# Kernel tuning notes

Measured on AMD Instinct MI355X. Metric: run time of the kernel, lower is better.

Reference implementation:

```python
import jax, jax.numpy as jnp
import numpy as np

N = 50000      # nodes
E = 800000     # edges (avg degree 16)
D = 128        # node_dim
H = 128        # hidden_dim
ED = 16        # edge_dim (unused by GCNConv, kept for signature fidelity)
G = 64         # graphs in batch
EPS = 1e-5     # BatchNorm eps


def setup_inputs() -> dict:
    key = jax.random.key(0)
    ks = jax.random.split(key, 16)
    s = 0.05
    inp = {
        "x": jax.random.normal(ks[0], (N, D), jnp.float32),
        "edge_index": jax.random.randint(ks[1], (2, E), 0, N, dtype=jnp.int64),
        "edge_attr": jax.random.normal(ks[2], (E, ED), jnp.float32),
        "batch": jnp.sort(jax.random.randint(ks[3], (N,), 0, G, dtype=jnp.int64)),
        # GCNConv weights/biases
        "W1": jax.random.normal(ks[4], (D, H), jnp.float32) * s,
        "b1": jnp.zeros((H,), jnp.float32),
        "W2": jax.random.normal(ks[5], (H, H), jnp.float32) * s,
        "b2": jnp.zeros((H,), jnp.float32),
        "W3": jax.random.normal(ks[6], (H, H), jnp.float32) * s,
        "b3": jnp.zeros((H,), jnp.float32),
        # BatchNorm affine params (training-mode batch stats)
        "g1": jnp.ones((H,), jnp.float32), "be1": jnp.zeros((H,), jnp.float32),
        "g2": jnp.ones((H,), jnp.float32), "be2": jnp.zeros((H,), jnp.float32),
        "g3": jnp.ones((H,), jnp.float32), "be3": jnp.zeros((H,), jnp.float32),
    }
    return inp


def reference(x, edge_index, edge_attr, batch,
              W1, b1, W2, b2, W3, b3,
              g1, be1, g2, be2, g3, be3):
    n = x.shape[0]
    src, dst = edge_index[0], edge_index[1]

    # GCN symmetric normalization with added self-loops:
    # deg[i] = 1 + in_degree(i); norm(e) = deg[src]^-1/2 * deg[dst]^-1/2
    deg = jax.ops.segment_sum(jnp.ones((src.shape[0],), x.dtype), dst,
                              num_segments=n) + 1.0
    dinv = jax.lax.rsqrt(deg)
    edge_norm = (dinv[src] * dinv[dst])[:, None]   # [E,1]
    self_norm = (dinv * dinv)[:, None]             # [N,1] self-loop weight

    def gcn(h, W, b):
        h = h @ W                                  # [N,H]
        agg = jax.ops.segment_sum(h[src] * edge_norm, dst, num_segments=n)
        return agg + h * self_norm + b

    def bn_sigmoid(h, g, b):
        m = h.mean(0)
        v = jnp.mean(jnp.square(h - m), 0)         # biased variance (torch BN)
        return jax.nn.sigmoid((h - m) * jax.lax.rsqrt(v + EPS) * g + b)

    h = bn_sigmoid(gcn(x, W1, b1), g1, be1)
    h = bn_sigmoid(gcn(h, W2, b2), g2, be2)
    h = bn_sigmoid(gcn(h, W3, b3), g3, be3)

    # global_mean_pool over graph ids
    cnt = jax.ops.segment_sum(jnp.ones((n,), h.dtype), batch, num_segments=G)
    pooled = jax.ops.segment_sum(h, batch, num_segments=G)
    return pooled / jnp.maximum(cnt, 1.0)[:, None]
```

## Files before the change

kernel.cpp:

```cpp
#include <hip/hip_runtime.h>
#include <math.h>

#define NDIM 128

typedef __attribute__((ext_vector_type(8))) short short8;
typedef __attribute__((ext_vector_type(4))) float f32x4;

__device__ __forceinline__ float sigmoidf_(float x){ return 1.0f/(1.0f + __expf(-x)); }

__device__ __forceinline__ unsigned short f2bf(float f){
  unsigned u = __float_as_uint(f);
  unsigned r = (u + 0x7fffu + ((u >> 16) & 1u)) >> 16;
  return (unsigned short)r;
}

__global__ void deg_count_k(const int* __restrict__ dst, int* __restrict__ counts, int E){
  int e = blockIdx.x*blockDim.x + threadIdx.x;
  if(e < E) atomicAdd(&counts[dst[e]], 1);
}

__global__ void scan1_k(const int* __restrict__ counts, int* __restrict__ scanned,
                        int* __restrict__ chunksums, int N){
  __shared__ int lds[256];
  int t = threadIdx.x; int idx = blockIdx.x*256 + t;
  int x = (idx < N) ? counts[idx] : 0;
  lds[t] = x; __syncthreads();
  for(int o=1;o<256;o<<=1){
    int v = (t>=o) ? lds[t-o] : 0;
    __syncthreads();
    lds[t] += v;
    __syncthreads();
  }
  if(idx < N) scanned[idx] = lds[t];
  if(t == 255) chunksums[blockIdx.x] = lds[255];
}

__global__ void scan2_k(int* __restrict__ chunksums, int nchunks){
  __shared__ int lds[256];
  int t = threadIdx.x;
  int x = (t < nchunks) ? chunksums[t] : 0;
  lds[t] = x; __syncthreads();
  for(int o=1;o<256;o<<=1){
    int v = (t>=o) ? lds[t-o] : 0;
    __syncthreads();
    lds[t] += v;
    __syncthreads();
  }
  if(t < nchunks) chunksums[t] = lds[t] - x;
}

__global__ void scan3_k(const int* __restrict__ scanned, const int* __restrict__ counts,
                        const int* __restrict__ chunksums, int* __restrict__ row_start,
                        float* __restrict__ dinv, int N){
  int i = blockIdx.x*blockDim.x + threadIdx.x;
  if(i < N){
    row_start[i] = scanned[i] - counts[i] + chunksums[i>>8];
    dinv[i] = rsqrtf(1.0f + (float)counts[i]);
  }
}

__global__ void fill_k(const int* __restrict__ src, const int* __restrict__ dst,
                       const float* __restrict__ dinv, const int* __restrict__ row_start,
                       int* __restrict__ cursor, uint2* __restrict__ csr, int E){
  int e = blockIdx.x*blockDim.x + threadIdx.x;
  if(e >= E) return;
  int d = dst[e], s = src[e];
  int pos = row_start[d] + atomicAdd(&cursor[d], 1);
  uint2 rec;
  rec.x = (unsigned)s;
  rec.y = __float_as_uint(dinv[s]*dinv[d]);
  csr[pos] = rec;
}

__global__ void bounds_k(const int* __restrict__ batch, int* __restrict__ bound, int N, int G){
  int g = threadIdx.x;
  if(g > G) return;
  int lo = 0, hi = N;
  while(lo < hi){ int mid = (lo+hi)>>1; if(batch[mid] < g) lo = mid+1; else hi = mid; }
  bound[g] = lo;
}

__global__ void wprep_k(const float* __restrict__ W0, const float* __restrict__ W1,
                        const float* __restrict__ W2, unsigned short* __restrict__ Wsw){
  int t = blockIdx.x*256 + threadIdx.x;
  if(t >= 3*16384) return;
  int l = t >> 14; int i = t & 16383;
  const float* W = (l==0) ? W0 : ((l==1) ? W1 : W2);
  int k = i >> 7, n = i & 127;
  Wsw[l*16384 + (((k>>3)*128 + n)<<3) + (k&7)] = f2bf(W[k*128+n]);
}

__global__ __launch_bounds__(256) void gemm_mfma_k(const float* __restrict__ A,
                                                   const unsigned short* __restrict__ Wsw,
                                                   unsigned short* __restrict__ Bh,
                                                   const float* __restrict__ scale,
                                                   const float* __restrict__ shift,
                                                   int N){
  __shared__ unsigned short Al[16384];
  __shared__ unsigned short Wl[16384];
  int t = threadIdx.x;
  int row0 = blockIdx.x * 128;
  bool bn = (scale != nullptr);

  #pragma unroll
  for(int i=0;i<8;i++){
    int u = t + i*256;
    *(uint4*)&Wl[u<<3] = *(const uint4*)&Wsw[u<<3];
  }
  int o = t & 15, rbase = t >> 4;
  #pragma unroll
  for(int it=0; it<8; it++){
    int r = rbase + it*16;
    int grow = row0 + r;
    float4 v0 = make_float4(0.f,0.f,0.f,0.f), v1 = v0;
    if(grow < N){
      v0 = *(const float4*)&A[grow*NDIM + o*8];
      v1 = *(const float4*)&A[grow*NDIM + o*8 + 4];
      if(bn){
        float4 sc0 = *(const float4*)&scale[o*8],   sh0 = *(const float4*)&shift[o*8];
        float4 sc1 = *(const float4*)&scale[o*8+4], sh1 = *(const float4*)&shift[o*8+4];
        v0.x = sigmoidf_(v0.x*sc0.x + sh0.x); v0.y = sigmoidf_(v0.y*sc0.y + sh0.y);
        v0.z = sigmoidf_(v0.z*sc0.z + sh0.z); v0.w = sigmoidf_(v0.w*sc0.w + sh0.w);
        v1.x = sigmoidf_(v1.x*sc1.x + sh1.x); v1.y = sigmoidf_(v1.y*sc1.y + sh1.y);
        v1.z = sigmoidf_(v1.z*sc1.z + sh1.z); v1.w = sigmoidf_(v1.w*sc1.w + sh1.w);
      }
    }
    uint4 pk;
    pk.x = (unsigned)f2bf(v0.x) | ((unsigned)f2bf(v0.y)<<16);
    pk.y = (unsigned)f2bf(v0.z) | ((unsigned)f2bf(v0.w)<<16);
    pk.z = (unsigned)f2bf(v1.x) | ((unsigned)f2bf(v1.y)<<16);
    pk.w = (unsigned)f2bf(v1.z) | ((unsigned)f2bf(v1.w)<<16);
    *(uint4*)&Al[(o*128 + r)<<3] = pk;
  }
  __syncthreads();

  int wv = t >> 6, lane = t & 63, quad = lane >> 4, l16 = lane & 15;
  int rw = (wv & 1) * 64, cw = (wv >> 1) * 64;
  f32x4 acc[4][4];
  #pragma unroll
  for(int rt=0;rt<4;rt++)
    #pragma unroll
    for(int ct=0;ct<4;ct++) acc[rt][ct] = (f32x4){0.f,0.f,0.f,0.f};

  #pragma unroll
  for(int ks=0; ks<4; ks++){
    short8 a[4], b[4];
    #pragma unroll
    for(int rt=0;rt<4;rt++)
      a[rt] = *(short8*)&Al[(((ks*4+quad)*128) + rw + rt*16 + l16) << 3];
    #pragma unroll
    for(int ct=0;ct<4;ct++)
      b[ct] = *(short8*)&Wl[(((ks*4+quad)*128) + cw + ct*16 + l16) << 3];
    #pragma unroll
    for(int rt=0;rt<4;rt++)
      #pragma unroll
      for(int ct=0;ct<4;ct++)
        acc[rt][ct] = __builtin_amdgcn_mfma_f32_16x16x32_bf16(a[rt], b[ct], acc[rt][ct], 0, 0, 0);
  }

  #pragma unroll
  for(int rt=0;rt<4;rt++){
    int gr = row0 + rw + rt*16 + quad*4;
    #pragma unroll
    for(int ct=0;ct<4;ct++){
      int col = cw + ct*16 + l16;
      #pragma unroll
      for(int reg=0;reg<4;reg++){
        if(gr + reg < N) Bh[(gr+reg)*NDIM + col] = f2bf(acc[rt][ct][reg]);
      }
    }
  }
}

__global__ void agg_k(const unsigned int* __restrict__ hb,
                      const float* __restrict__ dinv,
                      const int* __restrict__ row_start, const int* __restrict__ counts,
                      const uint2* __restrict__ csr,
                      const float* __restrict__ bias, float* __restrict__ hC, int N){
  int i = blockIdx.x;
  if(i >= N) return;
  int lane = threadIdx.x;
  int rs = row_start[i], re = rs + counts[i];
  float ax = 0.f, ay = 0.f;
  int j = rs;
  for(; j+3 < re; j += 4){
    uint2 r0 = csr[j], r1 = csr[j+1], r2 = csr[j+2], r3 = csr[j+3];
    unsigned u0 = hb[(size_t)r0.x*64 + lane];
    unsigned u1 = hb[(size_t)r1.x*64 + lane];
    unsigned u2 = hb[(size_t)r2.x*64 + lane];
    unsigned u3 = hb[(size_t)r3.x*64 + lane];
    float n0 = __uint_as_float(r0.y), n1 = __uint_as_float(r1.y);
    float n2 = __uint_as_float(r2.y), n3 = __uint_as_float(r3.y);
    ax += n0*__uint_as_float(u0<<16) + n1*__uint_as_float(u1<<16)
        + n2*__uint_as_float(u2<<16) + n3*__uint_as_float(u3<<16);
    ay += n0*__uint_as_float(u0 & 0xffff0000u) + n1*__uint_as_float(u1 & 0xffff0000u)
        + n2*__uint_as_float(u2 & 0xffff0000u) + n3*__uint_as_float(u3 & 0xffff0000u);
  }
  for(; j < re; j++){
    uint2 r0 = csr[j];
    unsigned u0 = hb[(size_t)r0.x*64 + lane];
    float n0 = __uint_as_float(r0.y);
    ax += n0*__uint_as_float(u0<<16);
    ay += n0*__uint_as_float(u0 & 0xffff0000u);
  }
  float di = dinv[i], sn = di*di;
  unsigned su = hb[(size_t)i*64 + lane];
  float2 bv = *(const float2*)&bias[lane*2];
  float2 o;
  o.x = ax + sn*__uint_as_float(su<<16)           + bv.x;
  o.y = ay + sn*__uint_as_float(su & 0xffff0000u) + bv.y;
  *(float2*)&hC[(size_t)i*NDIM + lane*2] = o;
}

__global__ void stats_k(const float* __restrict__ h, float* __restrict__ sums,
                        float* __restrict__ sumsq, int N){
  __shared__ float ls[256], lq[256];
  int t = threadIdx.x;
  int f = t & 127, half = t >> 7;
  int rowsPerBlock = (N + gridDim.x - 1)/gridDim.x;
  int r0 = blockIdx.x * rowsPerBlock;
  int r1 = min(N, r0 + rowsPerBlock);
  float s=0.f, q=0.f;
  for(int r=r0+half; r<r1; r+=2){
    float v = h[r*NDIM + f];
    s += v; q += v*v;
  }
  ls[t]=s; lq[t]=q; __syncthreads();
  if(t < 128){
    s = ls[t] + ls[t+128];
    q = lq[t] + lq[t+128];
    atomicAdd(&sums[f], s);
    atomicAdd(&sumsq[f], q);
  }
}

__global__ void finalize_k(const float* __restrict__ sums, const float* __restrict__ sumsq,
                           const float* __restrict__ g, const float* __restrict__ be,
                           float* __restrict__ scale, float* __restrict__ shift, int N){
  int f = threadIdx.x;
  float invN = 1.0f/(float)N;
  float m = sums[f]*invN;
  float var = fmaxf(sumsq[f]*invN - m*m, 0.f);
  float s = g[f]*rsqrtf(var + 1e-5f);
  scale[f] = s;
  shift[f] = be[f] - m*s;
}

#define PCH 128
__global__ __launch_bounds__(256) void pool_k(const float* __restrict__ hC,
                                              const int* __restrict__ batch,
                                              const float* __restrict__ scale,
                                              const float* __restrict__ shift,
                                              float* __restrict__ out, int N){
  int t = threadIdx.x;
  int f = t & 127, half = t >> 7;
  int r0 = blockIdx.x*PCH + half;
  int r1 = min(N, blockIdx.x*PCH + PCH);
  float sc = scale[f], sh = shift[f];
  float acc = 0.f; int cur = -1;
  for(int r = r0; r < r1; r += 2){
    int g = batch[r];
    if(g != cur){
      if(cur >= 0) atomicAdd(&out[cur*NDIM + f], acc);
      acc = 0.f; cur = g;
    }
    acc += sigmoidf_(hC[r*NDIM + f]*sc + sh);
  }
  if(cur >= 0) atomicAdd(&out[cur*NDIM + f], acc);
}

__global__ void div_k(float* __restrict__ out, const int* __restrict__ bound){
  int g = blockIdx.x, f = threadIdx.x;
  float cnt = (float)(bound[g+1] - bound[g]);
  out[g*NDIM + f] /= fmaxf(cnt, 1.0f);
}

extern "C" void kernel_launch(void* const* d_in, const int* in_sizes, int n_in,
                              void* d_out, int out_size, void* d_ws, size_t ws_size,
                              hipStream_t stream){
  const float* x     = (const float*)d_in[0];
  const int*   ei    = (const int*)d_in[1];
  const int*   batch = (const int*)d_in[3];
  const float* W [3] = {(const float*)d_in[4], (const float*)d_in[6], (const float*)d_in[8]};
  const float* bi[3] = {(const float*)d_in[5], (const float*)d_in[7], (const float*)d_in[9]};
  const float* gg[3] = {(const float*)d_in[10], (const float*)d_in[12], (const float*)d_in[14]};
  const float* bb[3] = {(const float*)d_in[11], (const float*)d_in[13], (const float*)d_in[15]};

  int N = in_sizes[0] / NDIM;
  int E = in_sizes[1] / 2;
  int G = out_size / NDIM;
  const int* src = ei;
  const int* dst = ei + E;

  char* p = (char*)d_ws;
  auto alloc = [&](size_t bytes)->void*{
    void* r = (void*)p; p += (bytes + 255) & ~(size_t)255; return r;
  };
  unsigned short* hB  = (unsigned short*)alloc((size_t)N*NDIM*2);
  unsigned short* Wsw = (unsigned short*)alloc(3*16384*2);
  float* hC        = (float*)alloc((size_t)N*NDIM*4);
  int*   counts    = (int*)  alloc((size_t)2*N*4);
  int*   cursor    = counts + N;
  int*   scanned   = (int*)  alloc((size_t)N*4);
  int*   chunksums = (int*)  alloc(256*4);
  int*   row_start = (int*)  alloc((size_t)N*4);
  float* dinv      = (float*)alloc((size_t)N*4);
  uint2* csr       = (uint2*)alloc((size_t)E*8);
  float* sums      = (float*)alloc(2*3*128*4);
  float* sumsq     = sums + 3*128;
  float* scale     = (float*)alloc(3*128*4);
  float* shift     = (float*)alloc(3*128*4);
  int*   bound     = (int*)  alloc(256*4);

  hipMemsetAsync(counts, 0, (size_t)2*N*4, stream);
  hipMemsetAsync(sums,  0, 2*3*128*4, stream);
  hipMemsetAsync(d_out, 0, (size_t)out_size*4, stream);

  deg_count_k<<<(E+255)/256, 256, 0, stream>>>(dst, counts, E);

  int nchunks = (N+255)/256;
  scan1_k<<<nchunks, 256, 0, stream>>>(counts, scanned, chunksums, N);
  scan2_k<<<1, 256, 0, stream>>>(chunksums, nchunks);
  scan3_k<<<(N+255)/256, 256, 0, stream>>>(scanned, counts, chunksums, row_start, dinv, N);
  fill_k<<<(E+255)/256, 256, 0, stream>>>(src, dst, dinv, row_start, cursor, csr, E);
  bounds_k<<<1, 128, 0, stream>>>(batch, bound, N, G);
  wprep_k<<<(3*16384+255)/256, 256, 0, stream>>>(W[0], W[1], W[2], Wsw);

  const float* hin = x;
  for(int l=0; l<3; l++){
    const float* sc = (l == 0) ? nullptr : (scale + (l-1)*128);
    const float* sh = (l == 0) ? nullptr : (shift + (l-1)*128);
    gemm_mfma_k<<<(N+127)/128, 256, 0, stream>>>(hin, Wsw + l*16384, hB, sc, sh, N);
    agg_k<<<N, 64, 0, stream>>>((const unsigned int*)hB, dinv, row_start, counts,
                                csr, bi[l], hC, N);
    stats_k<<<400, 256, 0, stream>>>(hC, sums + l*128, sumsq + l*128, N);
    finalize_k<<<1, 128, 0, stream>>>(sums + l*128, sumsq + l*128, gg[l], bb[l],
                                      scale + l*128, shift + l*128, N);
    hin = hC;
  }

  pool_k<<<(N+PCH-1)/PCH, 256, 0, stream>>>(hC, batch, scale + 2*128, shift + 2*128,
                                            (float*)d_out, N);
  div_k<<<G, 128, 0, stream>>>((float*)d_out, bound);
}
```

Measured before the change: 474.2 us.

## Fold GCN normalization into GEMM epilogue, compress CSR to 16-bit indices, fuse finalize

```diff
diff --git a/kernel.cpp b/kernel.cpp
--- a/kernel.cpp
+++ b/kernel.cpp
@@ -60,48 +60,64 @@
 }
 
 __global__ void fill_k(const int* __restrict__ src, const int* __restrict__ dst,
-                       const float* __restrict__ dinv, const int* __restrict__ row_start,
-                       int* __restrict__ cursor, uint2* __restrict__ csr, int E){
+                       const int* __restrict__ row_start,
+                       int* __restrict__ cursor, unsigned short* __restrict__ csr, int E){
   int e = blockIdx.x*blockDim.x + threadIdx.x;
   if(e >= E) return;
-  int d = dst[e], s = src[e];
+  int d = dst[e];
   int pos = row_start[d] + atomicAdd(&cursor[d], 1);
-  uint2 rec;
-  rec.x = (unsigned)s;
-  rec.y = __float_as_uint(dinv[s]*dinv[d]);
-  csr[pos] = rec;
-}
-
-__global__ void bounds_k(const int* __restrict__ batch, int* __restrict__ bound, int N, int G){
-  int g = threadIdx.x;
-  if(g > G) return;
-  int lo = 0, hi = N;
-  while(lo < hi){ int mid = (lo+hi)>>1; if(batch[mid] < g) lo = mid+1; else hi = mid; }
-  bound[g] = lo;
+  csr[pos] = (unsigned short)src[e];
 }
 
 __global__ void wprep_k(const float* __restrict__ W0, const float* __restrict__ W1,
-                        const float* __restrict__ W2, unsigned short* __restrict__ Wsw){
+                        const float* __restrict__ W2, unsigned short* __restrict__ Wsw,
+                        const int* __restrict__ batch, int* __restrict__ bound,
+                        int N, int G){
   int t = blockIdx.x*256 + threadIdx.x;
-  if(t >= 3*16384) return;
-  int l = t >> 14; int i = t & 16383;
-  const float* W = (l==0) ? W0 : ((l==1) ? W1 : W2);
-  int k = i >> 7, n = i & 127;
-  Wsw[l*16384 + (((k>>3)*128 + n)<<3) + (k&7)] = f2bf(W[k*128+n]);
+  if(t < 3*16384){
+    int l = t >> 14; int i = t & 16383;
+    const float* W = (l==0) ? W0 : ((l==1) ? W1 : W2);
+    int k = i >> 7, n = i & 127;
+    Wsw[l*16384 + (((k>>3)*128 + n)<<3) + (k&7)] = f2bf(W[k*128+n]);
+  } else {
+    int g = t - 3*16384;
+    if(g <= G){
+      int lo = 0, hi = N;
+      while(lo < hi){ int mid = (lo+hi)>>1; if(batch[mid] < g) lo = mid+1; else hi = mid; }
+      bound[g] = lo;
+    }
+  }
 }
 
 __global__ __launch_bounds__(256) void gemm_mfma_k(const float* __restrict__ A,
                                                    const unsigned short* __restrict__ Wsw,
                                                    unsigned short* __restrict__ Bh,
-                                                   const float* __restrict__ scale,
-                                                   const float* __restrict__ shift,
+                                                   const float* __restrict__ dinv,
+                                                   const float* __restrict__ sums,
+                                                   const float* __restrict__ sumsq,
+                                                   const float* __restrict__ gam,
+                                                   const float* __restrict__ bet,
                                                    int N){
   __shared__ unsigned short Al[16384];
   __shared__ unsigned short Wl[16384];
+  __shared__ float scl[NDIM], shl[NDIM], dvl[NDIM];
   int t = threadIdx.x;
   int row0 = blockIdx.x * 128;
-  bool bn = (scale != nullptr);
-
+  bool bn = (sums != nullptr);
+
+  if(bn && t < NDIM){
+    float invN = 1.0f/(float)N;
+    float m = sums[t]*invN;
+    float var = fmaxf(sumsq[t]*invN - m*m, 0.f);
+    float s = gam[t]*rsqrtf(var + 1e-5f);
+    scl[t] = s; shl[t] = bet[t] - m*s;
+  }
+  __syncthreads();
+
+  if(t < NDIM){
+    int r = row0 + t;
+    dvl[t] = (r < N) ? dinv[r] : 0.f;
+  }
   #pragma unroll
   for(int i=0;i<8;i++){
     int u = t + i*256;
@@ -117,8 +133,8 @@
       v0 = *(const float4*)&A[grow*NDIM + o*8];
       v1 = *(const float4*)&A[grow*NDIM + o*8 + 4];
       if(bn){
-        float4 sc0 = *(const float4*)&scale[o*8],   sh0 = *(const float4*)&shift[o*8];
-        float4 sc1 = *(const float4*)&scale[o*8+4], sh1 = *(const float4*)&shift[o*8+4];
+        float4 sc0 = *(const float4*)&scl[o*8],   sh0 = *(const float4*)&shl[o*8];
+        float4 sc1 = *(const float4*)&scl[o*8+4], sh1 = *(const float4*)&shl[o*8+4];
         v0.x = sigmoidf_(v0.x*sc0.x + sh0.x); v0.y = sigmoidf_(v0.y*sc0.y + sh0.y);
         v0.z = sigmoidf_(v0.z*sc0.z + sh0.z); v0.w = sigmoidf_(v0.w*sc0.w + sh0.w);
         v1.x = sigmoidf_(v1.x*sc1.x + sh1.x); v1.y = sigmoidf_(v1.y*sc1.y + sh1.y);
@@ -160,13 +176,17 @@
 
   #pragma unroll
   for(int rt=0;rt<4;rt++){
-    int gr = row0 + rw + rt*16 + quad*4;
-    #pragma unroll
-    for(int ct=0;ct<4;ct++){
-      int col = cw + ct*16 + l16;
-      #pragma unroll
-      for(int reg=0;reg<4;reg++){
-        if(gr + reg < N) Bh[(gr+reg)*NDIM + col] = f2bf(acc[rt][ct][reg]);
+    int lr = rw + rt*16 + quad*4;
+    int gr = row0 + lr;
+    #pragma unroll
+    for(int reg=0;reg<4;reg++){
+      float dv = dvl[lr + reg];
+      if(gr + reg < N){
+        #pragma unroll
+        for(int ct=0;ct<4;ct++){
+          int col = cw + ct*16 + l16;
+          Bh[(gr+reg)*NDIM + col] = f2bf(acc[rt][ct][reg]*dv);
+        }
       }
     }
   }
@@ -175,7 +195,7 @@
 __global__ void agg_k(const unsigned int* __restrict__ hb,
                       const float* __restrict__ dinv,
                       const int* __restrict__ row_start, const int* __restrict__ counts,
-                      const uint2* __restrict__ csr,
+                      const unsigned short* __restrict__ csr,
                       const float* __restrict__ bias, float* __restrict__ hC, int N){
   int i = blockIdx.x;
   if(i >= N) return;
@@ -183,32 +203,38 @@
   int rs = row_start[i], re = rs + counts[i];
   float ax = 0.f, ay = 0.f;
   int j = rs;
-  for(; j+3 < re; j += 4){
-    uint2 r0 = csr[j], r1 = csr[j+1], r2 = csr[j+2], r3 = csr[j+3];
-    unsigned u0 = hb[(size_t)r0.x*64 + lane];
-    unsigned u1 = hb[(size_t)r1.x*64 + lane];
-    unsigned u2 = hb[(size_t)r2.x*64 + lane];
-    unsigned u3 = hb[(size_t)r3.x*64 + lane];
-    float n0 = __uint_as_float(r0.y), n1 = __uint_as_float(r1.y);
-    float n2 = __uint_as_float(r2.y), n3 = __uint_as_float(r3.y);
-    ax += n0*__uint_as_float(u0<<16) + n1*__uint_as_float(u1<<16)
-        + n2*__uint_as_float(u2<<16) + n3*__uint_as_float(u3<<16);
-    ay += n0*__uint_as_float(u0 & 0xffff0000u) + n1*__uint_as_float(u1 & 0xffff0000u)
-        + n2*__uint_as_float(u2 & 0xffff0000u) + n3*__uint_as_float(u3 & 0xffff0000u);
+  for(; j+7 < re; j += 8){
+    int s0=csr[j],   s1=csr[j+1], s2=csr[j+2], s3=csr[j+3];
+    int s4=csr[j+4], s5=csr[j+5], s6=csr[j+6], s7=csr[j+7];
+    unsigned u0 = hb[(size_t)s0*64 + lane];
+    unsigned u1 = hb[(size_t)s1*64 + lane];
+    unsigned u2 = hb[(size_t)s2*64 + lane];
+    unsigned u3 = hb[(size_t)s3*64 + lane];
+    unsigned u4 = hb[(size_t)s4*64 + lane];
+    unsigned u5 = hb[(size_t)s5*64 + lane];
+    unsigned u6 = hb[(size_t)s6*64 + lane];
+    unsigned u7 = hb[(size_t)s7*64 + lane];
+    ax += __uint_as_float(u0<<16) + __uint_as_float(u1<<16)
+        + __uint_as_float(u2<<16) + __uint_as_float(u3<<16)
+        + __uint_as_float(u4<<16) + __uint_as_float(u5<<16)
+        + __uint_as_float(u6<<16) + __uint_as_float(u7<<16);
+    ay += __uint_as_float(u0 & 0xffff0000u) + __uint_as_float(u1 & 0xffff0000u)
+        + __uint_as_float(u2 & 0xffff0000u) + __uint_as_float(u3 & 0xffff0000u)
+        + __uint_as_float(u4 & 0xffff0000u) + __uint_as_float(u5 & 0xffff0000u)
+        + __uint_as_float(u6 & 0xffff0000u) + __uint_as_float(u7 & 0xffff0000u);
   }
   for(; j < re; j++){
-    uint2 r0 = csr[j];
-    unsigned u0 = hb[(size_t)r0.x*64 + lane];
-    float n0 = __uint_as_float(r0.y);
-    ax += n0*__uint_as_float(u0<<16);
-    ay += n0*__uint_as_float(u0 & 0xffff0000u);
-  }
-  float di = dinv[i], sn = di*di;
+    int s0 = csr[j];
+    unsigned u0 = hb[(size_t)s0*64 + lane];
+    ax += __uint_as_float(u0<<16);
+    ay += __uint_as_float(u0 & 0xffff0000u);
+  }
+  float di = dinv[i];
   unsigned su = hb[(size_t)i*64 + lane];
   float2 bv = *(const float2*)&bias[lane*2];
   float2 o;
-  o.x = ax + sn*__uint_as_float(su<<16)           + bv.x;
-  o.y = ay + sn*__uint_as_float(su & 0xffff0000u) + bv.y;
+  o.x = di*(ax + __uint_as_float(su<<16))           + bv.x;
+  o.y = di*(ay + __uint_as_float(su & 0xffff0000u)) + bv.y;
   *(float2*)&hC[(size_t)i*NDIM + lane*2] = o;
 }
 
@@ -234,29 +260,28 @@
   }
 }
 
-__global__ void finalize_k(const float* __restrict__ sums, const float* __restrict__ sumsq,
-                           const float* __restrict__ g, const float* __restrict__ be,
-                           float* __restrict__ scale, float* __restrict__ shift, int N){
-  int f = threadIdx.x;
-  float invN = 1.0f/(float)N;
-  float m = sums[f]*invN;
-  float var = fmaxf(sumsq[f]*invN - m*m, 0.f);
-  float s = g[f]*rsqrtf(var + 1e-5f);
-  scale[f] = s;
-  shift[f] = be[f] - m*s;
-}
-
 #define PCH 128
 __global__ __launch_bounds__(256) void pool_k(const float* __restrict__ hC,
                                               const int* __restrict__ batch,
-                                              const float* __restrict__ scale,
-                                              const float* __restrict__ shift,
+                                              const float* __restrict__ sums,
+                                              const float* __restrict__ sumsq,
+                                              const float* __restrict__ gam,
+                                              const float* __restrict__ bet,
                                               float* __restrict__ out, int N){
+  __shared__ float scl[NDIM], shl[NDIM];
   int t = threadIdx.x;
+  if(t < NDIM){
+    float invN = 1.0f/(float)N;
+    float m = sums[t]*invN;
+    float var = fmaxf(sumsq[t]*invN - m*m, 0.f);
+    float s = gam[t]*rsqrtf(var + 1e-5f);
+    scl[t] = s; shl[t] = bet[t] - m*s;
+  }
+  __syncthreads();
   int f = t & 127, half = t >> 7;
   int r0 = blockIdx.x*PCH + half;
   int r1 = min(N, blockIdx.x*PCH + PCH);
-  float sc = scale[f], sh = shift[f];
+  float sc = scl[f], sh = shl[f];
   float acc = 0.f; int cur = -1;
   for(int r = r0; r < r1; r += 2){
     int g = batch[r];
@@ -305,11 +330,9 @@
   int*   chunksums = (int*)  alloc(256*4);
   int*   row_start = (int*)  alloc((size_t)N*4);
   float* dinv      = (float*)alloc((size_t)N*4);
-  uint2* csr       = (uint2*)alloc((size_t)E*8);
+  unsigned short* csr = (unsigned short*)alloc((size_t)E*2);
   float* sums      = (float*)alloc(2*3*128*4);
   float* sumsq     = sums + 3*128;
-  float* scale     = (float*)alloc(3*128*4);
-  float* shift     = (float*)alloc(3*128*4);
   int*   bound     = (int*)  alloc(256*4);
 
   hipMemsetAsync(counts, 0, (size_t)2*N*4, stream);
@@ -322,24 +345,24 @@
   scan1_k<<<nchunks, 256, 0, stream>>>(counts, scanned, chunksums, N);
   scan2_k<<<1, 256, 0, stream>>>(chunksums, nchunks);
   scan3_k<<<(N+255)/256, 256, 0, stream>>>(scanned, counts, chunksums, row_start, dinv, N);
-  fill_k<<<(E+255)/256, 256, 0, stream>>>(src, dst, dinv, row_start, cursor, csr, E);
-  bounds_k<<<1, 128, 0, stream>>>(batch, bound, N, G);
-  wprep_k<<<(3*16384+255)/256, 256, 0, stream>>>(W[0], W[1], W[2], Wsw);
+  fill_k<<<(E+255)/256, 256, 0, stream>>>(src, dst, row_start, cursor, csr, E);
+  wprep_k<<<(3*16384+256+255)/256, 256, 0, stream>>>(W[0], W[1], W[2], Wsw, batch, bound, N, G);
 
   const float* hin = x;
   for(int l=0; l<3; l++){
-    const float* sc = (l == 0) ? nullptr : (scale + (l-1)*128);
-    const float* sh = (l == 0) ? nullptr : (shift + (l-1)*128);
-    gemm_mfma_k<<<(N+127)/128, 256, 0, stream>>>(hin, Wsw + l*16384, hB, sc, sh, N);
+    const float* sm = (l == 0) ? nullptr : (sums  + (l-1)*128);
+    const float* sq = (l == 0) ? nullptr : (sumsq + (l-1)*128);
+    const float* gm = (l == 0) ? nullptr : gg[l-1];
+    const float* be = (l == 0) ? nullptr : bb[l-1];
+    gemm_mfma_k<<<(N+127)/128, 256, 0, stream>>>(hin, Wsw + l*16384, hB, dinv,
+                                                 sm, sq, gm, be, N);
     agg_k<<<N, 64, 0, stream>>>((const unsigned int*)hB, dinv, row_start, counts,
                                 csr, bi[l], hC, N);
     stats_k<<<400, 256, 0, stream>>>(hC, sums + l*128, sumsq + l*128, N);
-    finalize_k<<<1, 128, 0, stream>>>(sums + l*128, sumsq + l*128, gg[l], bb[l],
-                                      scale + l*128, shift + l*128, N);
     hin = hC;
   }
 
-  pool_k<<<(N+PCH-1)/PCH, 256, 0, stream>>>(hC, batch, scale + 2*128, shift + 2*128,
-                                            (float*)d_out, N);
+  pool_k<<<(N+PCH-1)/PCH, 256, 0, stream>>>(hC, batch, sums + 2*128, sumsq + 2*128,
+                                            gg[2], bb[2], (float*)d_out, N);
   div_k<<<G, 128, 0, stream>>>((float*)d_out, bound);
 }
```

After: 475.7 us. Within noise of the previous version (+0.3%).
